# Optimization experiments

Measured on AMD Instinct MI355X. Metric: run time of the kernel, lower is better.

## Reference

```python
import jax, jax.numpy as jnp
import numpy as np

B, C, H, W = 2, 16, 160, 192
S, D = 3, 48
MIN_DEPTH, MAX_DEPTH = 0.5, 10.0
EPS = 1e-6


def setup_inputs() -> dict:
    key = jax.random.key(0)
    k1, k2 = jax.random.split(key)
    ref_feats = jax.random.normal(k1, (B, C, H, W), jnp.float32)
    src_feats = jax.random.normal(k2, (S, B, C, H, W), jnp.float32)
    K = np.array([[200.0, 0.0, W / 2.0], [0.0, 200.0, H / 2.0], [0.0, 0.0, 1.0]], np.float32)
    ref_intrinsics = jnp.broadcast_to(jnp.asarray(K), (B, 3, 3))
    src_intrinsics = jnp.broadcast_to(jnp.asarray(K), (S, B, 3, 3))
    T = np.tile(np.eye(4, dtype=np.float32), (S, B, 1, 1))
    T[:, :, 0, 3] = np.array([0.15, -0.15, 0.05], np.float32)[:, None]  # x baselines
    T[:, :, 1, 3] = 0.05  # small y offset
    ref_to_src = jnp.asarray(T)
    depth_hypotheses = jnp.linspace(MIN_DEPTH, MAX_DEPTH, D, dtype=jnp.float32)
    return {"ref_feats": ref_feats, "src_feats": src_feats,
            "ref_intrinsics": ref_intrinsics, "src_intrinsics": src_intrinsics,
            "ref_to_src": ref_to_src, "depth_hypotheses": depth_hypotheses}


def _bilinear(img, x, y, valid):
    """img: [B,C,Hs,Ws]; x,y,valid: [B,D,N]. Zero padding outside. -> [B,C,D,N]"""
    Hs, Ws = img.shape[2], img.shape[3]
    x0 = jnp.floor(x); y0 = jnp.floor(y)
    fx = x - x0; fy = y - y0
    x0i = x0.astype(jnp.int32); y0i = y0.astype(jnp.int32)
    gather = jax.vmap(lambda im, yy, xx: im[:, yy, xx])  # per-batch [C,D,N]
    out = jnp.zeros(img.shape[:2] + x.shape[1:], img.dtype)
    for dy in (0, 1):
        for dx in (0, 1):
            xi = x0i + dx; yi = y0i + dy
            w = (fx if dx else 1.0 - fx) * (fy if dy else 1.0 - fy)
            ok = valid & (xi >= 0) & (xi < Ws) & (yi >= 0) & (yi < Hs)
            vals = gather(img, jnp.clip(yi, 0, Hs - 1), jnp.clip(xi, 0, Ws - 1))
            out = out + vals * jnp.where(ok, w, 0.0)[:, None]
    return out


def _ncc(f1, f2, eps=EPS):
    """NCC over channel axis 1. f1: [B,C,1,H,W], f2: [B,C,D,H,W] -> [B,D,H,W]"""
    f1 = f1 - f1.mean(axis=1, keepdims=True)
    f2 = f2 - f2.mean(axis=1, keepdims=True)
    num = (f1 * f2).sum(axis=1)
    den = jnp.sqrt((f1 * f1).sum(axis=1)) * jnp.sqrt((f2 * f2).sum(axis=1)) + eps
    return num / den


def reference(ref_feats, src_feats, ref_intrinsics, src_intrinsics, ref_to_src, depth_hypotheses):
    b, c, h, w = ref_feats.shape
    s = src_feats.shape[0]
    us, vs = jnp.meshgrid(jnp.arange(w, dtype=jnp.float32), jnp.arange(h, dtype=jnp.float32))  # [h,w]
    pix = jnp.stack([us.ravel(), vs.ravel(), jnp.ones(h * w, jnp.float32)], axis=0)  # [3,HW]
    rays = jnp.einsum('bij,jn->bin', jnp.linalg.inv(ref_intrinsics), pix)  # [B,3,HW]
    X = depth_hypotheses[None, :, None, None] * rays[:, None]  # [B,D,3,HW]
    cost = jnp.zeros((b, depth_hypotheses.shape[0], h, w), ref_feats.dtype)
    for si in range(s):
        R = ref_to_src[si, :, :3, :3]; t = ref_to_src[si, :, :3, 3]
        Xs = jnp.einsum('bij,bdjn->bdin', R, X) + t[:, None, :, None]  # [B,D,3,HW]
        p = jnp.einsum('bij,bdjn->bdin', src_intrinsics[si], Xs)
        z = p[:, :, 2]
        valid = z > 1e-3
        zs = jnp.maximum(z, 1e-3)
        x = p[:, :, 0] / zs; y = p[:, :, 1] / zs  # [B,D,HW]
        warped = _bilinear(src_feats[si], x, y, valid).reshape(b, c, -1, h, w)  # [B,C,D,H,W]
        cost = cost + _ncc(ref_feats[:, :, None], warped)
    return cost / s
```

## Files before the change

### kernel.cpp

```cpp
#include <hip/hip_runtime.h>
#include <math.h>

constexpr int B = 2, C = 16, H = 160, W = 192, S = 3, D = 48;
constexpr int HW = H * W;
constexpr int SB = S * B;

__global__ void precompute_mats(const float* __restrict__ ref_intr,
                                const float* __restrict__ src_intr,
                                const float* __restrict__ ref_to_src,
                                double* __restrict__ ws)
{
    const int i = threadIdx.x;
    if (i >= SB) return;
    const int b = i % B;

    const float* Kp = ref_intr + b * 9;
    const double a00 = Kp[0], a01 = Kp[1], a02 = Kp[2];
    const double a10 = Kp[3], a11 = Kp[4], a12 = Kp[5];
    const double a20 = Kp[6], a21 = Kp[7], a22 = Kp[8];
    const double c00 =  (a11 * a22 - a12 * a21);
    const double c01 = -(a10 * a22 - a12 * a20);
    const double c02 =  (a10 * a21 - a11 * a20);
    const double c10 = -(a01 * a22 - a02 * a21);
    const double c11 =  (a00 * a22 - a02 * a20);
    const double c12 = -(a00 * a21 - a01 * a20);
    const double c20 =  (a01 * a12 - a02 * a11);
    const double c21 = -(a00 * a12 - a02 * a10);
    const double c22 =  (a00 * a11 - a01 * a10);
    const double invdet = 1.0 / (a00 * c00 + a01 * c01 + a02 * c02);
    const double iK[9] = { c00 * invdet, c10 * invdet, c20 * invdet,
                           c01 * invdet, c11 * invdet, c21 * invdet,
                           c02 * invdet, c12 * invdet, c22 * invdet };

    const float* Tp = ref_to_src + i * 16;
    const float* Ks = src_intr + i * 9;

    double M[9];
    #pragma unroll
    for (int r = 0; r < 3; ++r)
        #pragma unroll
        for (int c = 0; c < 3; ++c)
            M[r * 3 + c] = (double)Tp[r * 4 + 0] * iK[0 + c]
                         + (double)Tp[r * 4 + 1] * iK[3 + c]
                         + (double)Tp[r * 4 + 2] * iK[6 + c];

    double* o = ws + i * 12;
    #pragma unroll
    for (int r = 0; r < 3; ++r) {
        #pragma unroll
        for (int c = 0; c < 3; ++c)
            o[r * 3 + c] = (double)Ks[r * 3 + 0] * M[0 + c]
                         + (double)Ks[r * 3 + 1] * M[3 + c]
                         + (double)Ks[r * 3 + 2] * M[6 + c];
        o[9 + r] = (double)Ks[r * 3 + 0] * (double)Tp[3]
                 + (double)Ks[r * 3 + 1] * (double)Tp[7]
                 + (double)Ks[r * 3 + 2] * (double)Tp[11];
    }
}

__global__ __launch_bounds__(256) void plane_sweep_kernel(
    const float* __restrict__ ref_feats,
    const float* __restrict__ src_feats,
    const float* __restrict__ depths,
    const double* __restrict__ mats,
    float* __restrict__ out)
{
    const int pix = blockIdx.x * 256 + threadIdx.x;
    const int by  = blockIdx.y;
    const int d   = by % D;
    const int b   = by / D;

    const int w = pix % W;
    const int h = pix / W;

    const float* rb = ref_feats + (size_t)b * C * HW;
    float sum1 = 0.0f, sqr1 = 0.0f;
    #pragma unroll
    for (int c = 0; c < C; ++c) {
        const float rc = rb[c * HW + pix];
        sum1 += rc;
        sqr1 = fmaf(rc, rc, sqr1);
    }
    const float m1 = sum1 * (1.0f / C);
    float sq1 = fmaf(-sum1, m1, sqr1);
    sq1 = fmaxf(sq1, 0.0f);
    const float n1 = sqrtf(sq1);

    const double u = (double)w, v = (double)h;
    const double depth = (double)depths[d];
    float cost = 0.0f;

    #pragma unroll 1
    for (int s = 0; s < S; ++s) {
        const double* Aq = mats + (s * B + b) * 12;
        const double rx = fma(u, Aq[0], fma(v, Aq[1], Aq[2]));
        const double ry = fma(u, Aq[3], fma(v, Aq[4], Aq[5]));
        const double rz = fma(u, Aq[6], fma(v, Aq[7], Aq[8]));

        const double p0 = fma(depth, rx, Aq[9]);
        const double p1 = fma(depth, ry, Aq[10]);
        const double p2 = fma(depth, rz, Aq[11]);

        const bool valid = p2 > 0.001;
        const double zs = fmax(p2, 0.001);
#if __has_builtin(__builtin_amdgcn_rcp)
        double r = __builtin_amdgcn_rcp(zs);
#else
        double r = (double)__builtin_amdgcn_rcpf((float)zs);
        r = r * fma(-zs, r, 2.0);
#endif
        r = r * fma(-zs, r, 2.0);
        const double x = p0 * r;
        const double y = p1 * r;

        const double x0f = floor(x);
        const double y0f = floor(y);
        const float fx = (float)(x - x0f);
        const float fy = (float)(y - y0f);
        const int x0 = (int)x0f;
        const int y0 = (int)y0f;
        const int x1 = x0 + 1;
        const int y1 = y0 + 1;

        const float gx = 1.0f - fx, gy = 1.0f - fy;
        const bool okx0 = (x0 >= 0) & (x0 < W);
        const bool okx1 = (x1 >= 0) & (x1 < W);
        const bool oky0 = (y0 >= 0) & (y0 < H);
        const bool oky1 = (y1 >= 0) & (y1 < H);
        const float w00 = (valid & okx0 & oky0) ? gx * gy : 0.0f;
        const float w01 = (valid & okx1 & oky0) ? fx * gy : 0.0f;
        const float w10 = (valid & okx0 & oky1) ? gx * fy : 0.0f;
        const float w11 = (valid & okx1 & oky1) ? fx * fy : 0.0f;

        const int x0c = min(max(x0, 0), W - 1);
        const int x1c = min(max(x1, 0), W - 1);
        const int y0c = min(max(y0, 0), H - 1);
        const int y1c = min(max(y1, 0), H - 1);
        const int off00 = y0c * W + x0c;
        const int off01 = y0c * W + x1c;
        const int off10 = y1c * W + x0c;
        const int off11 = y1c * W + x1c;

        const float* sb = src_feats + (size_t)(s * B + b) * C * HW;

        float rdot, st = 0.0f, s2 = 0.0f, av;
        {
            const float rc = rb[pix];
            const float val = w00 * sb[off00] + w01 * sb[off01]
                            + w10 * sb[off10] + w11 * sb[off11];
            av = val;
            rdot = rc * val;
        }
        #pragma unroll
        for (int c = 1; c < C; ++c) {
            const float* p = sb + c * HW;
            const float rc = rb[c * HW + pix];
            const float v00 = p[off00];
            const float v01 = p[off01];
            const float v10 = p[off10];
            const float v11 = p[off11];
            const float val = w00 * v00 + w01 * v01 + w10 * v10 + w11 * v11;
            const float t = val - av;
            st += t;
            s2 = fmaf(t, t, s2);
            rdot = fmaf(rc, val, rdot);
        }
        const float sv = fmaf((float)C, av, st);
        const float dot = fmaf(-m1, sv, rdot);
        float sq2 = fmaf(-st * (1.0f / C), st, s2);
        sq2 = fmaxf(sq2, 0.0f);
        cost += dot / (n1 * sqrtf(sq2) + 1e-6f);
    }

    out[(size_t)by * HW + pix] = cost * (1.0f / S);
}

extern "C" void kernel_launch(void* const* d_in, const int* in_sizes, int n_in,
                              void* d_out, int out_size, void* d_ws, size_t ws_size,
                              hipStream_t stream) {
    const float* ref_feats  = (const float*)d_in[0];
    const float* src_feats  = (const float*)d_in[1];
    const float* ref_intr   = (const float*)d_in[2];
    const float* src_intr   = (const float*)d_in[3];
    const float* ref_to_src = (const float*)d_in[4];
    const float* depths     = (const float*)d_in[5];
    float* out = (float*)d_out;
    double* mats = (double*)d_ws;

    precompute_mats<<<1, 64, 0, stream>>>(ref_intr, src_intr, ref_to_src, mats);

    dim3 grid(HW / 256, B * D);
    plane_sweep_kernel<<<grid, dim3(256), 0, stream>>>(
        ref_feats, src_feats, depths, mats, out);
}
```

Baseline: 161.6 us.

## Fuse source-view loop into single channel loop, reading ref features once

Computes the bilinear geometry for all three source views up front, then walks the channels once, accumulating the NCC statistics for the three views and the reference mean/norm together. Previously the reference features were read four times per pixel (once for the norm, once per source view). Merging the loops also puts three independent gather streams in flight per iteration, which should hide load latency better. The cost is higher register pressure from holding twelve weights, twelve offsets and twelve accumulators, which may reduce occupancy.

```diff
diff --git a/kernel.cpp b/kernel.cpp
--- a/kernel.cpp
+++ b/kernel.cpp
@@ -73,26 +73,12 @@
     const int w = pix % W;
     const int h = pix / W;
 
-    const float* rb = ref_feats + (size_t)b * C * HW;
-    float sum1 = 0.0f, sqr1 = 0.0f;
-    #pragma unroll
-    for (int c = 0; c < C; ++c) {
-        const float rc = rb[c * HW + pix];
-        sum1 += rc;
-        sqr1 = fmaf(rc, rc, sqr1);
-    }
-    const float m1 = sum1 * (1.0f / C);
-    float sq1 = fmaf(-sum1, m1, sqr1);
-    sq1 = fmaxf(sq1, 0.0f);
-    const float n1 = sqrtf(sq1);
-
     const double u = (double)w, v = (double)h;
     const double depth = (double)depths[d];
-    float cost = 0.0f;
-
-    #pragma unroll 1
-    for (int s = 0; s < S; ++s) {
-        const double* Aq = mats + (s * B + b) * 12;
+
+    auto geom = [&](const double* Aq,
+                    float& w00, float& w01, float& w10, float& w11,
+                    int& o00, int& o01, int& o10, int& o11) {
         const double rx = fma(u, Aq[0], fma(v, Aq[1], Aq[2]));
         const double ry = fma(u, Aq[3], fma(v, Aq[4], Aq[5]));
         const double rz = fma(u, Aq[6], fma(v, Aq[7], Aq[8]));
@@ -127,47 +113,108 @@
         const bool okx1 = (x1 >= 0) & (x1 < W);
         const bool oky0 = (y0 >= 0) & (y0 < H);
         const bool oky1 = (y1 >= 0) & (y1 < H);
-        const float w00 = (valid & okx0 & oky0) ? gx * gy : 0.0f;
-        const float w01 = (valid & okx1 & oky0) ? fx * gy : 0.0f;
-        const float w10 = (valid & okx0 & oky1) ? gx * fy : 0.0f;
-        const float w11 = (valid & okx1 & oky1) ? fx * fy : 0.0f;
+        w00 = (valid & okx0 & oky0) ? gx * gy : 0.0f;
+        w01 = (valid & okx1 & oky0) ? fx * gy : 0.0f;
+        w10 = (valid & okx0 & oky1) ? gx * fy : 0.0f;
+        w11 = (valid & okx1 & oky1) ? fx * fy : 0.0f;
 
         const int x0c = min(max(x0, 0), W - 1);
         const int x1c = min(max(x1, 0), W - 1);
         const int y0c = min(max(y0, 0), H - 1);
         const int y1c = min(max(y1, 0), H - 1);
-        const int off00 = y0c * W + x0c;
-        const int off01 = y0c * W + x1c;
-        const int off10 = y1c * W + x0c;
-        const int off11 = y1c * W + x1c;
-
-        const float* sb = src_feats + (size_t)(s * B + b) * C * HW;
-
-        float rdot, st = 0.0f, s2 = 0.0f, av;
-        {
-            const float rc = rb[pix];
-            const float val = w00 * sb[off00] + w01 * sb[off01]
-                            + w10 * sb[off10] + w11 * sb[off11];
-            av = val;
-            rdot = rc * val;
-        }
-        #pragma unroll
-        for (int c = 1; c < C; ++c) {
-            const float* p = sb + c * HW;
-            const float rc = rb[c * HW + pix];
-            const float v00 = p[off00];
-            const float v01 = p[off01];
-            const float v10 = p[off10];
-            const float v11 = p[off11];
-            const float val = w00 * v00 + w01 * v01 + w10 * v10 + w11 * v11;
-            const float t = val - av;
-            st += t;
-            s2 = fmaf(t, t, s2);
-            rdot = fmaf(rc, val, rdot);
-        }
-        const float sv = fmaf((float)C, av, st);
-        const float dot = fmaf(-m1, sv, rdot);
-        float sq2 = fmaf(-st * (1.0f / C), st, s2);
+        o00 = y0c * W + x0c;
+        o01 = y0c * W + x1c;
+        o10 = y1c * W + x0c;
+        o11 = y1c * W + x1c;
+    };
+
+    float wa00, wa01, wa10, wa11; int oa00, oa01, oa10, oa11;
+    float wb00, wb01, wb10, wb11; int ob00, ob01, ob10, ob11;
+    float wc00, wc01, wc10, wc11; int oc00, oc01, oc10, oc11;
+    geom(mats + (0 * B + b) * 12, wa00, wa01, wa10, wa11, oa00, oa01, oa10, oa11);
+    geom(mats + (1 * B + b) * 12, wb00, wb01, wb10, wb11, ob00, ob01, ob10, ob11);
+    geom(mats + (2 * B + b) * 12, wc00, wc01, wc10, wc11, oc00, oc01, oc10, oc11);
+
+    const float* rb  = ref_feats + (size_t)b * C * HW;
+    const float* sb0 = src_feats + (size_t)(0 * B + b) * C * HW;
+    const float* sb1 = src_feats + (size_t)(1 * B + b) * C * HW;
+    const float* sb2 = src_feats + (size_t)(2 * B + b) * C * HW;
+
+    float sum1, sqr1;
+    float av0, st0 = 0.0f, s20 = 0.0f, rdot0;
+    float av1, st1 = 0.0f, s21 = 0.0f, rdot1;
+    float av2, st2 = 0.0f, s22 = 0.0f, rdot2;
+    {
+        const float rc = rb[pix];
+        sum1 = rc;
+        sqr1 = rc * rc;
+        const float v0 = wa00 * sb0[oa00] + wa01 * sb0[oa01]
+                       + wa10 * sb0[oa10] + wa11 * sb0[oa11];
+        const float v1 = wb00 * sb1[ob00] + wb01 * sb1[ob01]
+                       + wb10 * sb1[ob10] + wb11 * sb1[ob11];
+        const float v2 = wc00 * sb2[oc00] + wc01 * sb2[oc01]
+                       + wc10 * sb2[oc10] + wc11 * sb2[oc11];
+        av0 = v0; av1 = v1; av2 = v2;
+        rdot0 = rc * v0;
+        rdot1 = rc * v1;
+        rdot2 = rc * v2;
+    }
+    #pragma unroll 5
+    for (int c = 1; c < C; ++c) {
+        const float rc = rb[c * HW + pix];
+        sum1 += rc;
+        sqr1 = fmaf(rc, rc, sqr1);
+
+        const float* p0 = sb0 + c * HW;
+        const float* p1 = sb1 + c * HW;
+        const float* p2 = sb2 + c * HW;
+        const float val0 = wa00 * p0[oa00] + wa01 * p0[oa01]
+                         + wa10 * p0[oa10] + wa11 * p0[oa11];
+        const float val1 = wb00 * p1[ob00] + wb01 * p1[ob01]
+                         + wb10 * p1[ob10] + wb11 * p1[ob11];
+        const float val2 = wc00 * p2[oc00] + wc01 * p2[oc01]
+                         + wc10 * p2[oc10] + wc11 * p2[oc11];
+
+        const float t0 = val0 - av0;
+        st0 += t0;
+        s20 = fmaf(t0, t0, s20);
+        rdot0 = fmaf(rc, val0, rdot0);
+
+        const float t1 = val1 - av1;
+        st1 += t1;
+        s21 = fmaf(t1, t1, s21);
+        rdot1 = fmaf(rc, val1, rdot1);
+
+        const float t2 = val2 - av2;
+        st2 += t2;
+        s22 = fmaf(t2, t2, s22);
+        rdot2 = fmaf(rc, val2, rdot2);
+    }
+
+    const float m1 = sum1 * (1.0f / C);
+    float sq1 = fmaf(-sum1, m1, sqr1);
+    sq1 = fmaxf(sq1, 0.0f);
+    const float n1 = sqrtf(sq1);
+
+    float cost = 0.0f;
+    {
+        const float sv = fmaf((float)C, av0, st0);
+        const float dot = fmaf(-m1, sv, rdot0);
+        float sq2 = fmaf(-st0 * (1.0f / C), st0, s20);
+        sq2 = fmaxf(sq2, 0.0f);
+        cost += dot / (n1 * sqrtf(sq2) + 1e-6f);
+    }
+    {
+        const float sv = fmaf((float)C, av1, st1);
+        const float dot = fmaf(-m1, sv, rdot1);
+        float sq2 = fmaf(-st1 * (1.0f / C), st1, s21);
+        sq2 = fmaxf(sq2, 0.0f);
+        cost += dot / (n1 * sqrtf(sq2) + 1e-6f);
+    }
+    {
+        const float sv = fmaf((float)C, av2, st2);
+        const float dot = fmaf(-m1, sv, rdot2);
+        float sq2 = fmaf(-st2 * (1.0f / C), st2, s22);
         sq2 = fmaxf(sq2, 0.0f);
         cost += dot / (n1 * sqrtf(sq2) + 1e-6f);
     }
```

New measurement: 202.0 us. 1.25x slower.
